# Kernel tuning notes

Hardware: AMD Instinct MI355X
Metric: run time of the kernel (lower is better)

The kernel has to match this reference:

```python
import jax, jax.numpy as jnp
import numpy as np

H = 2048          # hidden_size
NH = 32           # num_attention_heads
NKV = 8           # num_key_value_heads
HD = H // NH      # head_dim = 64
GROUPS = NH // NKV
B, S = 1, 4096


def setup_inputs() -> dict:
    key = jax.random.key(0)
    k1, k2, k3, k4, k5 = jax.random.split(key, 5)
    hidden_states = jax.random.normal(k1, (B, S, H), dtype=jnp.float32)
    # additive causal mask [B, 1, S, S]
    causal = jnp.tril(jnp.ones((S, S), dtype=bool))
    attention_mask = jnp.where(causal, 0.0, jnp.finfo(jnp.float32).min)[None, None].astype(jnp.float32)
    scale = 0.02
    Wq = jax.random.normal(k2, (H, H), dtype=jnp.float32) * scale
    Wk = jax.random.normal(k3, (NKV * HD, H), dtype=jnp.float32) * scale
    Wv = jax.random.normal(k4, (NKV * HD, H), dtype=jnp.float32) * scale
    Wo = jax.random.normal(k5, (H, H), dtype=jnp.float32) * scale
    return {"hidden_states": hidden_states, "attention_mask": attention_mask,
            "Wq": Wq, "Wk": Wk, "Wv": Wv, "Wo": Wo}


def reference(hidden_states, attention_mask, Wq, Wk, Wv, Wo):
    bsz, q_len, _ = hidden_states.shape
    # projections (nn.Linear: x @ W.T)
    q = (hidden_states @ Wq.T).reshape(bsz, q_len, NH, HD).transpose(0, 2, 1, 3)   # [B,NH,S,HD]
    k = (hidden_states @ Wk.T).reshape(bsz, q_len, NKV, HD).transpose(0, 2, 1, 3)  # [B,NKV,S,HD]
    v = (hidden_states @ Wv.T).reshape(bsz, q_len, NKV, HD).transpose(0, 2, 1, 3)
    # repeat_kv: expand each KV head GROUPS times
    k = jnp.repeat(k, GROUPS, axis=1)  # [B,NH,S,HD]
    v = jnp.repeat(v, GROUPS, axis=1)
    attn_weights = jnp.einsum('bhqd,bhkd->bhqk', q, k) / jnp.sqrt(jnp.float32(HD))
    attn_weights = attn_weights + attention_mask
    attn_weights = jax.nn.softmax(attn_weights.astype(jnp.float32), axis=-1).astype(q.dtype)
    attn_output = jnp.einsum('bhqk,bhkd->bhqd', attn_weights, v)
    attn_output = attn_output.transpose(0, 2, 1, 3).reshape(bsz, q_len, H)
    return attn_output @ Wo.T
```

## Files before the change

kernel.cpp:

```cpp
#include <hip/hip_runtime.h>
#include <stdint.h>

#define S_LEN  4096
#define HDIM   2048
#define NHEADS 32
#define NKVH   8
#define HDSZ   64
#define KVDIM  (NKVH * HDSZ)
#define QKN    (HDIM + KVDIM)

typedef __bf16 v8bf16 __attribute__((ext_vector_type(8)));
typedef short  v4s    __attribute__((ext_vector_type(4)));
typedef float  v4f32  __attribute__((ext_vector_type(4)));

__device__ __forceinline__ unsigned short f2bf(float f) {
    uint32_t u = __builtin_bit_cast(uint32_t, f);
    uint32_t r = (u + 0x7fffu + ((u >> 16) & 1u)) >> 16;
    return (unsigned short)r;
}

__device__ __forceinline__ uint32_t pack_bf16(float a, float b) {
#if __has_builtin(__builtin_amdgcn_cvt_pk_bf16_f32)
    auto r = __builtin_amdgcn_cvt_pk_bf16_f32(a, b);
    return __builtin_bit_cast(uint32_t, r);
#else
    uint32_t ua = __builtin_bit_cast(uint32_t, a) + 0x8000u;
    uint32_t ub = __builtin_bit_cast(uint32_t, b) + 0x8000u;
    return (ua >> 16) | (ub & 0xffff0000u);
#endif
}

__device__ __forceinline__ float fast_exp2(float x) {
#if __has_builtin(__builtin_amdgcn_exp2f)
    return __builtin_amdgcn_exp2f(x);
#else
    float r; asm("v_exp_f32 %0, %1" : "=v"(r) : "v"(x)); return r;
#endif
}

__device__ __forceinline__ void async_load16(const void* g, void* l) {
    __builtin_amdgcn_global_load_lds((const __attribute__((address_space(1))) void*)g,
                                     (__attribute__((address_space(3))) void*)l,
                                     16, 0, 0);
}

#define SEG0 2097152
#define SEG1 3145728
#define SEG2 3407872
#define SEG3 3670016
#define SEGT 4718592
__global__ void cvt_all(const float* __restrict__ x,  const float* __restrict__ wq,
                        const float* __restrict__ wk, const float* __restrict__ wv,
                        const float* __restrict__ wo,
                        ushort4* __restrict__ xb, ushort4* __restrict__ wqkb,
                        ushort4* __restrict__ wvb, ushort4* __restrict__ wob,
                        float qscale)
{
    int i = blockIdx.x * blockDim.x + threadIdx.x;
    if (i >= SEGT) return;
    const float4* src; ushort4* dst; float s = 1.0f; int loc;
    if (i < SEG0)      { src = (const float4*)x;  dst = xb;   loc = i; }
    else if (i < SEG1) { src = (const float4*)wq; dst = wqkb; loc = i - SEG0; s = qscale; }
    else if (i < SEG2) { src = (const float4*)wk; dst = wqkb + 1048576; loc = i - SEG1; }
    else if (i < SEG3) { src = (const float4*)wv; dst = wvb;  loc = i - SEG2; }
    else               { src = (const float4*)wo; dst = wob;  loc = i - SEG3; }
    float4 f = src[loc];
    uint2 o;
    o.x = pack_bf16(f.x * s, f.y * s);
    o.y = pack_bf16(f.z * s, f.w * s);
    dst[loc] = __builtin_bit_cast(ushort4, o);
}


#define STAGE_A(buf, kh, t)                                                       \
    do {                                                                          \
        async_load16(A + aBase + (size_t)(t) * 64 + (kh) * 32,                    \
                     &smem[(buf) * 16384 + (kh) * 8192 + ldsSt]);                 \
        async_load16(A + aBase + (size_t)128 * Kd + (size_t)(t) * 64 + (kh) * 32, \
                     &smem[(buf) * 16384 + (kh) * 8192 + ldsSt + 4096]);          \
    } while (0)
#define STAGE_B(buf, kh, t)                                                       \
    do {                                                                          \
        async_load16(Bp + bBase + (size_t)(t) * 64 + (kh) * 32,                   \
                     &smem[32768 + (buf) * 16384 + (kh) * 8192 + ldsSt]);         \
        async_load16(Bp + bBase + (size_t)128 * Kd + (size_t)(t) * 64 + (kh) * 32,\
                     &smem[32768 + (buf) * 16384 + (kh) * 8192 + ldsSt + 4096]);  \
    } while (0)

#define LOAD_AF(khoff)                                                            \
    do {                                                                          \
        _Pragma("unroll")                                                         \
        for (int mi = 0; mi < 8; ++mi)                                            \
            af[mi] = *(const v8bf16*)&smem[curA + (khoff) + aRd + mi * 512];      \
    } while (0)

#define MFMA_PAIR(khoff, NI)                                                      \
    do {                                                                          \
        v8bf16 _b0 = *(const v8bf16*)&smem[curB + (khoff) + bRd + (NI) * 512];    \
        v8bf16 _b1 = *(const v8bf16*)&smem[curB + (khoff) + bRd + (NI) * 512 + 512];\
        __builtin_amdgcn_s_setprio(1);                                            \
        _Pragma("unroll")                                                         \
        for (int mi = 0; mi < 8; ++mi) {                                          \
            acc[mi][(NI)]     = __builtin_amdgcn_mfma_f32_16x16x32_bf16(af[mi], _b0, acc[mi][(NI)], 0, 0, 0);     \
            acc[mi][(NI) + 1] = __builtin_amdgcn_mfma_f32_16x16x32_bf16(af[mi], _b1, acc[mi][(NI) + 1], 0, 0, 0); \
        }                                                                         \
        __builtin_amdgcn_s_setprio(0);                                            \
    } while (0)

#define FENCE_BAR()                                                               \
    do {                                                                          \
        __builtin_amdgcn_sched_barrier(0);                                        \
        __builtin_amdgcn_s_barrier();                                             \
        __builtin_amdgcn_sched_barrier(0);                                        \
    } while (0)

#define WAITV(N) asm volatile("s_waitcnt vmcnt(" #N ")" ::: "memory")

template<bool F32OUT>
__device__ __forceinline__ void gemm256_body(
    const unsigned short* __restrict__ A,
    const unsigned short* __restrict__ Bp,
    void* __restrict__ Cout, int Nn, int Kd, int m0, int n0,
    unsigned short* __restrict__ smem)
{
    const int tid  = threadIdx.x;
    const int wave = tid >> 6;
    const int lane = tid & 63;
    const int lrow = lane & 15;
    const int quad = lane >> 4;
    const int wm = (wave >> 2) * 128;
    const int wn = (wave & 3) * 64;

    const int lr   = lane >> 2;
    const int sg4  = (lane & 3) ^ ((lane >> 3) & 3);
    const size_t aBase = (size_t)(m0 + wave * 16 + lr) * Kd + sg4 * 8;
    const size_t bBase = (size_t)(n0 + wave * 16 + lr) * Kd + sg4 * 8;
    const int ldsSt = wave * 512;

    const int rg4 = (quad ^ ((lrow >> 1) & 3)) * 8;
    const int aRd = (wm + lrow) * 32 + rg4;
    const int bRd = (wn + lrow) * 32 + rg4;

    const int NT = Kd >> 6;

    v4f32 acc[8][4];
#pragma unroll
    for (int mi = 0; mi < 8; ++mi)
#pragma unroll
        for (int ni = 0; ni < 4; ++ni)
#pragma unroll
            for (int r = 0; r < 4; ++r) acc[mi][ni][r] = 0.0f;

    STAGE_A(0, 0, 0); STAGE_B(0, 0, 0);
    STAGE_A(0, 1, 0); STAGE_B(0, 1, 0);
    STAGE_A(1, 0, 1); STAGE_B(1, 0, 1);
    WAITV(8);
    __builtin_amdgcn_s_barrier();
    __builtin_amdgcn_sched_barrier(0);

    v8bf16 af[8];
    for (int t = 0; t < NT - 2; ++t) {
        const int cur  = t & 1;
        const int nxt  = cur ^ 1;
        const int curA = cur * 16384;
        const int curB = 32768 + cur * 16384;

        STAGE_A(nxt, 1, t + 1);
        LOAD_AF(0);
        MFMA_PAIR(0, 0);
        FENCE_BAR();

        STAGE_B(nxt, 1, t + 1);
        MFMA_PAIR(0, 2);
        WAITV(8);
        FENCE_BAR();

        STAGE_A(cur, 0, t + 2);
        LOAD_AF(8192);
        MFMA_PAIR(8192, 0);
        FENCE_BAR();

        STAGE_B(cur, 0, t + 2);
        MFMA_PAIR(8192, 2);
        WAITV(8);
        FENCE_BAR();
    }

    {
        const int t = NT - 2;
        const int cur  = t & 1;
        const int nxt  = cur ^ 1;
        const int curA = cur * 16384;
        const int curB = 32768 + cur * 16384;

        STAGE_A(nxt, 1, t + 1);
        LOAD_AF(0);
        MFMA_PAIR(0, 0);
        FENCE_BAR();

        STAGE_B(nxt, 1, t + 1);
        MFMA_PAIR(0, 2);
        WAITV(8);
        FENCE_BAR();

        LOAD_AF(8192);
        MFMA_PAIR(8192, 0);
        FENCE_BAR();

        MFMA_PAIR(8192, 2);
        WAITV(4);
        FENCE_BAR();
    }

    {
        const int cur  = (NT - 1) & 1;
        const int curA = cur * 16384;
        const int curB = 32768 + cur * 16384;

        LOAD_AF(0);
        MFMA_PAIR(0, 0);
        FENCE_BAR();

        MFMA_PAIR(0, 2);
        WAITV(0);
        FENCE_BAR();

        LOAD_AF(8192);
        MFMA_PAIR(8192, 0);
        FENCE_BAR();

        MFMA_PAIR(8192, 2);
    }

    if (F32OUT) {
        float* Cf = (float*)Cout;
#pragma unroll
        for (int mi = 0; mi < 8; ++mi)
#pragma unroll
            for (int ni = 0; ni < 4; ++ni)
#pragma unroll
                for (int r = 0; r < 4; ++r) {
                    const int row = m0 + wm + mi * 16 + quad * 4 + r;
                    const int col = n0 + wn + ni * 16 + lrow;
                    Cf[(size_t)row * Nn + col] = acc[mi][ni][r];
                }
    } else {
        unsigned short* Cb = (unsigned short*)Cout;
#pragma unroll
        for (int mi = 0; mi < 8; ++mi)
#pragma unroll
            for (int ni = 0; ni < 4; ++ni)
#pragma unroll
                for (int r = 0; r < 4; ++r) {
                    const int row = m0 + wm + mi * 16 + quad * 4 + r;
                    const int col = n0 + wn + ni * 16 + lrow;
                    Cb[(size_t)row * Nn + col] = f2bf(acc[mi][ni][r]);
                }
    }
}

__global__ __launch_bounds__(512, 2)
void gemm_qkv256(const unsigned short* __restrict__ xb,
                 const unsigned short* __restrict__ Wqkb,
                 const unsigned short* __restrict__ Wvb,
                 unsigned short* __restrict__ QKb,
                 unsigned short* __restrict__ Vtb)
{
    __shared__ __align__(16) unsigned short smem[65536];
    const int bid = blockIdx.x;
    if (bid < 32) {
        gemm256_body<false>(Wvb, xb, Vtb, S_LEN, HDIM,
                            (bid >> 4) * 256, (bid & 15) * 256, smem);
    } else {
        const int b = bid - 32;
        gemm256_body<false>(xb, Wqkb, QKb, QKN, HDIM,
                            (b & 15) * 256, (b >> 4) * 256, smem);
    }
}


#define STAGE2_A(buf, kh, t)                                                      \
    async_load16(A + aBase + (size_t)(t) * 64 + (kh) * 32,                        \
                 &smem[(buf) * 8192 + (kh) * 4096 + ldsSt])
#define STAGE2_B(buf, kh, t)                                                      \
    do {                                                                          \
        async_load16(Bp + bBase + (size_t)(t) * 64 + (kh) * 32,                   \
                     &smem[16384 + (buf) * 16384 + (kh) * 8192 + ldsSt]);         \
        async_load16(Bp + bBase + (size_t)128 * 2048 + (size_t)(t) * 64 + (kh) * 32,\
                     &smem[16384 + (buf) * 16384 + (kh) * 8192 + ldsSt + 4096]);  \
    } while (0)

#define LOAD_AF2(khoff)                                                           \
    do {                                                                          \
        _Pragma("unroll")                                                         \
        for (int mi = 0; mi < 4; ++mi)                                            \
            af[mi] = *(const v8bf16*)&smem[curA + (khoff) + aRd + mi * 512];      \
    } while (0)

#define MFMA_PAIR2(khoff, NI)                                                     \
    do {                                                                          \
        v8bf16 _b0 = *(const v8bf16*)&smem[curB + (khoff) + bRd + (NI) * 512];    \
        v8bf16 _b1 = *(const v8bf16*)&smem[curB + (khoff) + bRd + (NI) * 512 + 512];\
        __builtin_amdgcn_s_setprio(1);                                            \
        _Pragma("unroll")                                                         \
        for (int mi = 0; mi < 4; ++mi) {                                          \
            acc[mi][(NI)]     = __builtin_amdgcn_mfma_f32_16x16x32_bf16(af[mi], _b0, acc[mi][(NI)], 0, 0, 0);     \
            acc[mi][(NI) + 1] = __builtin_amdgcn_mfma_f32_16x16x32_bf16(af[mi], _b1, acc[mi][(NI) + 1], 0, 0, 0); \
        }                                                                         \
        __builtin_amdgcn_s_setprio(0);                                            \
    } while (0)

__global__ __launch_bounds__(512, 1)
void gemm_o128(const unsigned short* __restrict__ A,
               const unsigned short* __restrict__ Bp,
               float* __restrict__ Cout)
{
    __shared__ __align__(16) unsigned short smem[49152];
    const int tid  = threadIdx.x;
    const int wave = tid >> 6;
    const int lane = tid & 63;
    const int lrow = lane & 15;
    const int quad = lane >> 4;
    const int wmi = wave >> 2;
    const int wni = wave & 3;

    const int m0 = (blockIdx.x >> 3) * 128;
    const int n0 = (blockIdx.x & 7) * 256;

    const int lr   = lane >> 2;
    const int sg4  = (lane & 3) ^ ((lane >> 3) & 3);
    const size_t aBase = (size_t)(m0 + wave * 16 + lr) * 2048 + sg4 * 8;
    const size_t bBase = (size_t)(n0 + wave * 16 + lr) * 2048 + sg4 * 8;
    const int ldsSt = wave * 512;

    const int rg4 = (quad ^ ((lrow >> 1) & 3)) * 8;
    const int aRd = (wmi * 64 + lrow) * 32 + rg4;
    const int bRd = (wni * 64 + lrow) * 32 + rg4;

    const int NT = 32;

    v4f32 acc[4][4];
#pragma unroll
    for (int mi = 0; mi < 4; ++mi)
#pragma unroll
        for (int ni = 0; ni < 4; ++ni)
#pragma unroll
            for (int r = 0; r < 4; ++r) acc[mi][ni][r] = 0.0f;

    STAGE2_A(0, 0, 0); STAGE2_B(0, 0, 0);
    STAGE2_A(0, 1, 0); STAGE2_B(0, 1, 0);
    STAGE2_A(1, 0, 1); STAGE2_B(1, 0, 1);
    WAITV(6);
    __builtin_amdgcn_s_barrier();
    __builtin_amdgcn_sched_barrier(0);

    v8bf16 af[4];
    for (int t = 0; t < NT - 2; ++t) {
        const int cur  = t & 1;
        const int nxt  = cur ^ 1;
        const int curA = cur * 8192;
        const int curB = 16384 + cur * 16384;

        STAGE2_A(nxt, 1, t + 1);
        LOAD_AF2(0);
        MFMA_PAIR2(0, 0);
        FENCE_BAR();

        STAGE2_B(nxt, 1, t + 1);
        MFMA_PAIR2(0, 2);
        WAITV(6);
        FENCE_BAR();

        STAGE2_A(cur, 0, t + 2);
        LOAD_AF2(4096);
        MFMA_PAIR2(8192, 0);
        FENCE_BAR();

        STAGE2_B(cur, 0, t + 2);
        MFMA_PAIR2(8192, 2);
        WAITV(6);
        FENCE_BAR();
    }

    {
        const int t = NT - 2;
        const int cur  = t & 1;
        const int nxt  = cur ^ 1;
        const int curA = cur * 8192;
        const int curB = 16384 + cur * 16384;

        STAGE2_A(nxt, 1, t + 1);
        LOAD_AF2(0);
        MFMA_PAIR2(0, 0);
        FENCE_BAR();

        STAGE2_B(nxt, 1, t + 1);
        MFMA_PAIR2(0, 2);
        WAITV(6);
        FENCE_BAR();

        LOAD_AF2(4096);
        MFMA_PAIR2(8192, 0);
        FENCE_BAR();

        MFMA_PAIR2(8192, 2);
        WAITV(3);
        FENCE_BAR();
    }

    {
        const int cur  = (NT - 1) & 1;
        const int curA = cur * 8192;
        const int curB = 16384 + cur * 16384;

        LOAD_AF2(0);
        MFMA_PAIR2(0, 0);
        FENCE_BAR();

        MFMA_PAIR2(0, 2);
        WAITV(0);
        FENCE_BAR();

        LOAD_AF2(4096);
        MFMA_PAIR2(8192, 0);
        FENCE_BAR();

        MFMA_PAIR2(8192, 2);
    }

#pragma unroll
    for (int mi = 0; mi < 4; ++mi)
#pragma unroll
        for (int ni = 0; ni < 4; ++ni)
#pragma unroll
            for (int r = 0; r < 4; ++r) {
                const int row = m0 + wmi * 64 + mi * 16 + quad * 4 + r;
                const int col = n0 + wni * 64 + ni * 16 + lrow;
                Cout[(size_t)row * HDIM + col] = acc[mi][ni][r];
            }
}

__global__ __launch_bounds__(256, 3)
void flash_attn(const unsigned short* __restrict__ QK,
                const unsigned short* __restrict__ Vt,
                unsigned short* __restrict__ O)
{
    __shared__ unsigned short smem[24576];
    unsigned short* Qs = smem;

    const int tid  = threadIdx.x;
    const int wave = tid >> 6;
    const int lane = tid & 63;
    const int lrow = lane & 15;
    const int quad = lane >> 4;

    const int h   = blockIdx.x;
    const int kvh = h >> 2;
    const int q0  = (gridDim.y - 1 - blockIdx.y) * 128;

    const int srow8 = lane >> 3;
    const int sgrp  = (lane & 7) ^ srow8;
    const v8bf16 v_one8 = __builtin_bit_cast(v8bf16,
        (uint4){0x3F803F80u, 0x3F803F80u, 0x3F803F80u, 0x3F803F80u});

    {
        const size_t gq = (size_t)(q0 + wave * 32 + srow8) * QKN + h * HDSZ + sgrp * 8;
#pragma unroll
        for (int i = 0; i < 4; ++i)
            async_load16(QK + gq + (size_t)(i * 8) * QKN, &Qs[(wave * 32 + i * 8) * 64]);
    }

    int kperm[2];
#pragma unroll
    for (int i = 0; i < 2; ++i) {
        const int slot = wave * 16 + i * 8 + srow8;
        const int nj = slot >> 4, sm = slot & 15;
        kperm[i] = 32 * (nj >> 1) + 8 * (sm >> 2) + 4 * (nj & 1) + (sm & 3);
    }

    auto stage_kv = [&](int j) {
        const int k0b = j * 64;
        const int buf = (j & 1) * 4096;
#pragma unroll
        for (int i = 0; i < 2; ++i) {
            const size_t gk = (size_t)(k0b + kperm[i]) * QKN
                              + HDIM + kvh * HDSZ + sgrp * 8;
            async_load16(QK + gk, &smem[8192 + buf + (wave * 16 + i * 8) * 64]);
        }
        const size_t gv = (size_t)(kvh * HDSZ + wave * 16 + srow8) * S_LEN
                          + k0b + sgrp * 8;
        async_load16(Vt + gv,             &smem[16384 + buf + (wave * 16) * 64]);
        async_load16(Vt + gv + 8 * S_LEN, &smem[16384 + buf + (wave * 16 + 8) * 64]);
    };

    v4f32 o_acc[2][4], l_acc[2];
#pragma unroll
    for (int mi = 0; mi < 2; ++mi) {
#pragma unroll
        for (int r = 0; r < 4; ++r) l_acc[mi][r] = 0.0f;
#pragma unroll
        for (int dj = 0; dj < 4; ++dj)
#pragma unroll
            for (int r = 0; r < 4; ++r) o_acc[mi][dj][r] = 0.0f;
    }

    const int rbase = q0 + wave * 32;
    const int njt   = (q0 >> 6) + 2;

    stage_kv(0);

    WAITV(4);
    __builtin_amdgcn_sched_barrier(0);
    v8bf16 qreg[2][2];
#pragma unroll
    for (int kk = 0; kk < 2; ++kk) {
        const int swz = ((kk * 4 + quad) ^ (lrow & 7)) * 8;
        qreg[kk][0] = *(const v8bf16*)&Qs[(wave * 32 + lrow) * 64 + swz];
        qreg[kk][1] = *(const v8bf16*)&Qs[(wave * 32 + 16 + lrow) * 64 + swz];
    }

    for (int j = 0; j < njt; ++j) {
        const int k0  = j * 64;
        const int buf = (j & 1) * 4096;

        if (j + 1 < njt) { stage_kv(j + 1); WAITV(4); }
        else             { WAITV(0); }
        __builtin_amdgcn_sched_barrier(0);
        __builtin_amdgcn_s_barrier();
        __builtin_amdgcn_sched_barrier(0);

        if (k0 <= rbase + 31) {
            const unsigned short* Ks = &smem[8192 + buf];
            const unsigned short* Vs = &smem[16384 + buf];

            v4f32 st[2][4];
#pragma unroll
            for (int mi = 0; mi < 2; ++mi)
#pragma unroll
                for (int nj = 0; nj < 4; ++nj)
#pragma unroll
                    for (int r = 0; r < 4; ++r) st[mi][nj][r] = 0.0f;
#pragma unroll
            for (int kk = 0; kk < 2; ++kk) {
                const int swz = ((kk * 4 + quad) ^ (lrow & 7)) * 8;
                __builtin_amdgcn_s_setprio(1);
#pragma unroll
                for (int nj = 0; nj < 4; ++nj) {
                    const v8bf16 kb = *(const v8bf16*)&Ks[(nj * 16 + lrow) * 64 + swz];
                    st[0][nj] = __builtin_amdgcn_mfma_f32_16x16x32_bf16(kb, qreg[kk][0], st[0][nj], 0, 0, 0);
                    st[1][nj] = __builtin_amdgcn_mfma_f32_16x16x32_bf16(kb, qreg[kk][1], st[1][nj], 0, 0, 0);
                }
                __builtin_amdgcn_s_setprio(0);
            }

            if (k0 + 63 > rbase) {
#pragma unroll
                for (int mi = 0; mi < 2; ++mi) {
                    const int qi = rbase + mi * 16 + lrow;
#pragma unroll
                    for (int nj = 0; nj < 4; ++nj) {
                        const int kib = k0 + 32 * (nj >> 1) + 8 * quad + 4 * (nj & 1);
#pragma unroll
                        for (int r = 0; r < 4; ++r)
                            if (kib + r > qi) st[mi][nj][r] = -1e30f;
                    }
                }
            }

            v8bf16 pk8[2][2];
#pragma unroll
            for (int mi = 0; mi < 2; ++mi) {
                uint2 pu[4];
#pragma unroll
                for (int nj = 0; nj < 4; ++nj) {
                    const float p0 = fast_exp2(st[mi][nj][0]);
                    const float p1 = fast_exp2(st[mi][nj][1]);
                    const float p2 = fast_exp2(st[mi][nj][2]);
                    const float p3 = fast_exp2(st[mi][nj][3]);
                    pu[nj].x = pack_bf16(p0, p1);
                    pu[nj].y = pack_bf16(p2, p3);
                }
                pk8[mi][0] = __builtin_bit_cast(v8bf16, (uint4){pu[0].x, pu[0].y, pu[1].x, pu[1].y});
                pk8[mi][1] = __builtin_bit_cast(v8bf16, (uint4){pu[2].x, pu[2].y, pu[3].x, pu[3].y});
            }

#pragma unroll
            for (int t = 0; t < 2; ++t) {
                const int swzv = ((t * 4 + quad) ^ (lrow & 7)) * 8;
                v8bf16 va[4];
#pragma unroll
                for (int dj = 0; dj < 4; ++dj)
                    va[dj] = *(const v8bf16*)&Vs[(dj * 16 + lrow) * 64 + swzv];
                __builtin_amdgcn_s_setprio(1);
#pragma unroll
                for (int dj = 0; dj < 4; ++dj) {
                    o_acc[0][dj] = __builtin_amdgcn_mfma_f32_16x16x32_bf16(va[dj], pk8[0][t], o_acc[0][dj], 0, 0, 0);
                    o_acc[1][dj] = __builtin_amdgcn_mfma_f32_16x16x32_bf16(va[dj], pk8[1][t], o_acc[1][dj], 0, 0, 0);
                }
                l_acc[0] = __builtin_amdgcn_mfma_f32_16x16x32_bf16(v_one8, pk8[0][t], l_acc[0], 0, 0, 0);
                l_acc[1] = __builtin_amdgcn_mfma_f32_16x16x32_bf16(v_one8, pk8[1][t], l_acc[1], 0, 0, 0);
                __builtin_amdgcn_s_setprio(0);
            }
        }

        __builtin_amdgcn_sched_barrier(0);
        __builtin_amdgcn_s_barrier();
        __builtin_amdgcn_sched_barrier(0);
    }

    __syncthreads();
    unsigned short* Os = smem;
#pragma unroll
    for (int mi = 0; mi < 2; ++mi) {
        const float inv = 1.0f / l_acc[mi][0];
#pragma unroll
        for (int dj = 0; dj < 4; ++dj)
#pragma unroll
            for (int r = 0; r < 4; ++r)
                Os[(wave * 32 + mi * 16 + lrow) * 72 + dj * 16 + quad * 4 + r] =
                    f2bf(o_acc[mi][dj][r] * inv);
    }
    __syncthreads();
#pragma unroll
    for (int i = 0; i < 4; ++i) {
        const int idx = i * 256 + tid;
        const int row = idx >> 3, c8 = idx & 7;
        const uint4 vv = *(const uint4*)&Os[row * 72 + c8 * 8];
        *(uint4*)&O[(size_t)(q0 + row) * HDIM + h * HDSZ + c8 * 8] = vv;
    }
}

extern "C" void kernel_launch(void* const* d_in, const int* in_sizes, int n_in,
                              void* d_out, int out_size, void* d_ws, size_t ws_size,
                              hipStream_t stream)
{
    const float* x  = (const float*)d_in[0];
    const float* Wq = (const float*)d_in[2];
    const float* Wk = (const float*)d_in[3];
    const float* Wv = (const float*)d_in[4];
    const float* Wo = (const float*)d_in[5];
    float* out = (float*)d_out;

    unsigned short* xb   = (unsigned short*)d_ws;
    unsigned short* Wqkb = xb   + (size_t)S_LEN * HDIM;
    unsigned short* Wvb  = Wqkb + (size_t)QKN * HDIM;
    unsigned short* Wob  = Wvb  + (size_t)KVDIM * HDIM;
    unsigned short* QKb  = Wob  + (size_t)HDIM * HDIM;
    unsigned short* Vtb  = QKb  + (size_t)S_LEN * QKN;
    unsigned short* AOb  = xb;

    cvt_all<<<(SEGT + 255) / 256, 256, 0, stream>>>(
        x, Wq, Wk, Wv, Wo,
        (ushort4*)xb, (ushort4*)Wqkb, (ushort4*)Wvb, (ushort4*)Wob,
        0.18033688011f);

    gemm_qkv256<<<192, 512, 0, stream>>>(xb, Wqkb, Wvb, QKb, Vtb);

    flash_attn<<<dim3(NHEADS, S_LEN / 128), 256, 0, stream>>>(QKb, Vtb, AOb);

    gemm_o128<<<256, 512, 0, stream>>>(AOb, Wob, out);
}
```

Baseline: 326.4 us.

## Software-pipeline attention loop: overlap QK^T of tile j with PV of tile j-1

Restructures the flash-attention inner loop so that each iteration computes the S=QK^T MFMAs for the current KV tile and then runs the P·V MFMAs for the previous tile, while the softmax exponentials for the current tile are issued afterwards. V gets a triple-buffered LDS ring so the previous tile's V stays resident while the next one is prefetched. P fragments ping-pong between two register sets, and a final PV drain runs after the loop. The goal is to hide exp/pack VALU latency behind independent MFMA work. The cost is more registers and LDS, plus a loop unrolled by two that relies on njt being even.

```diff
diff --git a/kernel.cpp b/kernel.cpp
--- a/kernel.cpp
+++ b/kernel.cpp
@@ -478,19 +478,25 @@
         kperm[i] = 32 * (nj >> 1) + 8 * (sm >> 2) + 4 * (nj & 1) + (sm & 3);
     }
 
+    auto voff = [](int j) -> int {
+        const int m = j % 3;
+        return m == 0 ? 16384 : (m == 1 ? 20480 : 0);
+    };
+
     auto stage_kv = [&](int j) {
         const int k0b = j * 64;
-        const int buf = (j & 1) * 4096;
+        const int kb  = 8192 + (j & 1) * 4096;
+        const int vb  = voff(j);
 #pragma unroll
         for (int i = 0; i < 2; ++i) {
             const size_t gk = (size_t)(k0b + kperm[i]) * QKN
                               + HDIM + kvh * HDSZ + sgrp * 8;
-            async_load16(QK + gk, &smem[8192 + buf + (wave * 16 + i * 8) * 64]);
+            async_load16(QK + gk, &smem[kb + (wave * 16 + i * 8) * 64]);
         }
         const size_t gv = (size_t)(kvh * HDSZ + wave * 16 + srow8) * S_LEN
                           + k0b + sgrp * 8;
-        async_load16(Vt + gv,             &smem[16384 + buf + (wave * 16) * 64]);
-        async_load16(Vt + gv + 8 * S_LEN, &smem[16384 + buf + (wave * 16 + 8) * 64]);
+        async_load16(Vt + gv,             &smem[vb + (wave * 16) * 64]);
+        async_load16(Vt + gv + 8 * S_LEN, &smem[vb + (wave * 16 + 8) * 64]);
     };
 
     v4f32 o_acc[2][4], l_acc[2];
@@ -506,6 +512,7 @@
 
     const int rbase = q0 + wave * 32;
     const int njt   = (q0 >> 6) + 2;
+    const int lastj = min(njt - 1, (rbase + 31) >> 6);
 
     stage_kv(0);
 
@@ -519,94 +526,107 @@
         qreg[kk][1] = *(const v8bf16*)&Qs[(wave * 32 + 16 + lrow) * 64 + swz];
     }
 
-    for (int j = 0; j < njt; ++j) {
-        const int k0  = j * 64;
-        const int buf = (j & 1) * 4096;
-
-        if (j + 1 < njt) { stage_kv(j + 1); WAITV(4); }
-        else             { WAITV(0); }
-        __builtin_amdgcn_sched_barrier(0);
-        __builtin_amdgcn_s_barrier();
-        __builtin_amdgcn_sched_barrier(0);
-
-        if (k0 <= rbase + 31) {
-            const unsigned short* Ks = &smem[8192 + buf];
-            const unsigned short* Vs = &smem[16384 + buf];
-
-            v4f32 st[2][4];
-#pragma unroll
-            for (int mi = 0; mi < 2; ++mi)
-#pragma unroll
-                for (int nj = 0; nj < 4; ++nj)
-#pragma unroll
-                    for (int r = 0; r < 4; ++r) st[mi][nj][r] = 0.0f;
-#pragma unroll
-            for (int kk = 0; kk < 2; ++kk) {
-                const int swz = ((kk * 4 + quad) ^ (lrow & 7)) * 8;
-                __builtin_amdgcn_s_setprio(1);
-#pragma unroll
-                for (int nj = 0; nj < 4; ++nj) {
-                    const v8bf16 kb = *(const v8bf16*)&Ks[(nj * 16 + lrow) * 64 + swz];
-                    st[0][nj] = __builtin_amdgcn_mfma_f32_16x16x32_bf16(kb, qreg[kk][0], st[0][nj], 0, 0, 0);
-                    st[1][nj] = __builtin_amdgcn_mfma_f32_16x16x32_bf16(kb, qreg[kk][1], st[1][nj], 0, 0, 0);
-                }
-                __builtin_amdgcn_s_setprio(0);
-            }
-
-            if (k0 + 63 > rbase) {
-#pragma unroll
-                for (int mi = 0; mi < 2; ++mi) {
-                    const int qi = rbase + mi * 16 + lrow;
-#pragma unroll
-                    for (int nj = 0; nj < 4; ++nj) {
-                        const int kib = k0 + 32 * (nj >> 1) + 8 * quad + 4 * (nj & 1);
-#pragma unroll
-                        for (int r = 0; r < 4; ++r)
-                            if (kib + r > qi) st[mi][nj][r] = -1e30f;
-                    }
-                }
-            }
-
-            v8bf16 pk8[2][2];
-#pragma unroll
-            for (int mi = 0; mi < 2; ++mi) {
-                uint2 pu[4];
-#pragma unroll
-                for (int nj = 0; nj < 4; ++nj) {
-                    const float p0 = fast_exp2(st[mi][nj][0]);
-                    const float p1 = fast_exp2(st[mi][nj][1]);
-                    const float p2 = fast_exp2(st[mi][nj][2]);
-                    const float p3 = fast_exp2(st[mi][nj][3]);
-                    pu[nj].x = pack_bf16(p0, p1);
-                    pu[nj].y = pack_bf16(p2, p3);
-                }
-                pk8[mi][0] = __builtin_bit_cast(v8bf16, (uint4){pu[0].x, pu[0].y, pu[1].x, pu[1].y});
-                pk8[mi][1] = __builtin_bit_cast(v8bf16, (uint4){pu[2].x, pu[2].y, pu[3].x, pu[3].y});
-            }
-
-#pragma unroll
-            for (int t = 0; t < 2; ++t) {
-                const int swzv = ((t * 4 + quad) ^ (lrow & 7)) * 8;
-                v8bf16 va[4];
-#pragma unroll
-                for (int dj = 0; dj < 4; ++dj)
-                    va[dj] = *(const v8bf16*)&Vs[(dj * 16 + lrow) * 64 + swzv];
-                __builtin_amdgcn_s_setprio(1);
-#pragma unroll
-                for (int dj = 0; dj < 4; ++dj) {
-                    o_acc[0][dj] = __builtin_amdgcn_mfma_f32_16x16x32_bf16(va[dj], pk8[0][t], o_acc[0][dj], 0, 0, 0);
-                    o_acc[1][dj] = __builtin_amdgcn_mfma_f32_16x16x32_bf16(va[dj], pk8[1][t], o_acc[1][dj], 0, 0, 0);
-                }
-                l_acc[0] = __builtin_amdgcn_mfma_f32_16x16x32_bf16(v_one8, pk8[0][t], l_acc[0], 0, 0, 0);
-                l_acc[1] = __builtin_amdgcn_mfma_f32_16x16x32_bf16(v_one8, pk8[1][t], l_acc[1], 0, 0, 0);
-                __builtin_amdgcn_s_setprio(0);
-            }
-        }
-
-        __builtin_amdgcn_sched_barrier(0);
-        __builtin_amdgcn_s_barrier();
-        __builtin_amdgcn_sched_barrier(0);
-    }
+    v8bf16 pkA[2][2], pkB[2][2];
+
+#define FA_PV(PKR, JPREV)                                                         \
+    do {                                                                          \
+        const unsigned short* Vs = &smem[voff(JPREV)];                            \
+        _Pragma("unroll")                                                         \
+        for (int t = 0; t < 2; ++t) {                                             \
+            const int swzv = ((t * 4 + quad) ^ (lrow & 7)) * 8;                   \
+            v8bf16 va[4];                                                         \
+            _Pragma("unroll")                                                     \
+            for (int dj = 0; dj < 4; ++dj)                                        \
+                va[dj] = *(const v8bf16*)&Vs[(dj * 16 + lrow) * 64 + swzv];       \
+            __builtin_amdgcn_s_setprio(1);                                        \
+            _Pragma("unroll")                                                     \
+            for (int dj = 0; dj < 4; ++dj) {                                      \
+                o_acc[0][dj] = __builtin_amdgcn_mfma_f32_16x16x32_bf16(va[dj], PKR[0][t], o_acc[0][dj], 0, 0, 0); \
+                o_acc[1][dj] = __builtin_amdgcn_mfma_f32_16x16x32_bf16(va[dj], PKR[1][t], o_acc[1][dj], 0, 0, 0); \
+            }                                                                     \
+            l_acc[0] = __builtin_amdgcn_mfma_f32_16x16x32_bf16(v_one8, PKR[0][t], l_acc[0], 0, 0, 0); \
+            l_acc[1] = __builtin_amdgcn_mfma_f32_16x16x32_bf16(v_one8, PKR[1][t], l_acc[1], 0, 0, 0); \
+            __builtin_amdgcn_s_setprio(0);                                        \
+        }                                                                         \
+    } while (0)
+
+#define FA_BODY(J, PKW, PKR)                                                      \
+    do {                                                                          \
+        const int k0 = (J) * 64;                                                  \
+        if ((J) + 1 < njt) { stage_kv((J) + 1); WAITV(4); }                       \
+        else               { WAITV(0); }                                          \
+        __builtin_amdgcn_sched_barrier(0);                                        \
+        __builtin_amdgcn_s_barrier();                                             \
+        __builtin_amdgcn_sched_barrier(0);                                        \
+        const bool qk_valid = (k0 <= rbase + 31);                                 \
+        const bool pv_valid = ((J) >= 1) && (((J) - 1) * 64 <= rbase + 31);       \
+        v4f32 st[2][4];                                                           \
+        if (qk_valid) {                                                           \
+            const unsigned short* Ks = &smem[8192 + ((J) & 1) * 4096];            \
+            _Pragma("unroll")                                                     \
+            for (int mi = 0; mi < 2; ++mi)                                        \
+                _Pragma("unroll")                                                 \
+                for (int nj = 0; nj < 4; ++nj)                                    \
+                    _Pragma("unroll")                                             \
+                    for (int r = 0; r < 4; ++r) st[mi][nj][r] = 0.0f;             \
+            _Pragma("unroll")                                                     \
+            for (int kk = 0; kk < 2; ++kk) {                                      \
+                const int swz = ((kk * 4 + quad) ^ (lrow & 7)) * 8;               \
+                __builtin_amdgcn_s_setprio(1);                                    \
+                _Pragma("unroll")                                                 \
+                for (int nj = 0; nj < 4; ++nj) {                                  \
+                    const v8bf16 kb = *(const v8bf16*)&Ks[(nj * 16 + lrow) * 64 + swz]; \
+                    st[0][nj] = __builtin_amdgcn_mfma_f32_16x16x32_bf16(kb, qreg[kk][0], st[0][nj], 0, 0, 0); \
+                    st[1][nj] = __builtin_amdgcn_mfma_f32_16x16x32_bf16(kb, qreg[kk][1], st[1][nj], 0, 0, 0); \
+                }                                                                 \
+                __builtin_amdgcn_s_setprio(0);                                    \
+            }                                                                     \
+        }                                                                         \
+        if (pv_valid) FA_PV(PKR, (J) - 1);                                        \
+        if (qk_valid) {                                                           \
+            if (k0 + 63 > rbase) {                                                \
+                _Pragma("unroll")                                                 \
+                for (int mi = 0; mi < 2; ++mi) {                                  \
+                    const int qi = rbase + mi * 16 + lrow;                        \
+                    _Pragma("unroll")                                             \
+                    for (int nj = 0; nj < 4; ++nj) {                              \
+                        const int kib = k0 + 32 * (nj >> 1) + 8 * quad + 4 * (nj & 1); \
+                        _Pragma("unroll")                                         \
+                        for (int r = 0; r < 4; ++r)                               \
+                            if (kib + r > qi) st[mi][nj][r] = -1e30f;             \
+                    }                                                             \
+                }                                                                 \
+            }                                                                     \
+            _Pragma("unroll")                                                     \
+            for (int mi = 0; mi < 2; ++mi) {                                      \
+                uint2 pu[4];                                                      \
+                _Pragma("unroll")                                                 \
+                for (int nj = 0; nj < 4; ++nj) {                                  \
+                    const float p0 = fast_exp2(st[mi][nj][0]);                    \
+                    const float p1 = fast_exp2(st[mi][nj][1]);                    \
+                    const float p2 = fast_exp2(st[mi][nj][2]);                    \
+                    const float p3 = fast_exp2(st[mi][nj][3]);                    \
+                    pu[nj].x = pack_bf16(p0, p1);                                 \
+                    pu[nj].y = pack_bf16(p2, p3);                                 \
+                }                                                                 \
+                PKW[mi][0] = __builtin_bit_cast(v8bf16, (uint4){pu[0].x, pu[0].y, pu[1].x, pu[1].y}); \
+                PKW[mi][1] = __builtin_bit_cast(v8bf16, (uint4){pu[2].x, pu[2].y, pu[3].x, pu[3].y}); \
+            }                                                                     \
+        }                                                                         \
+        __builtin_amdgcn_sched_barrier(0);                                        \
+        __builtin_amdgcn_s_barrier();                                             \
+        __builtin_amdgcn_sched_barrier(0);                                        \
+    } while (0)
+
+    for (int j = 0; j < njt; j += 2) {
+        FA_BODY(j, pkA, pkB);
+        FA_BODY(j + 1, pkB, pkA);
+    }
+
+    if (lastj == njt - 1) FA_PV(pkB, njt - 1);
+
+#undef FA_BODY
+#undef FA_PV
 
     __syncthreads();
     unsigned short* Os = smem;
```

After: 699.0 us. +114.2%, slower.
